# Performance work log

Measured on AMD Instinct MI355X. Metric: run time of the kernel, lower is better.

Reference implementation:

```python
import jax, jax.numpy as jnp
import numpy as np

ELEMENTS = (1, 6, 7, 8)
SIGMA = 3.0
NTRANSFORMS = 2


def fwht(x):
    """Fast Walsh-Hadamard transform over the last axis (unnormalized, d power of 2)."""
    d = x.shape[-1]
    lead = x.shape[:-1]
    x = x.reshape((-1, d))
    h = 1
    while h < d:
        x = x.reshape((-1, d // (2 * h), 2, h))
        a, b = x[..., 0, :], x[..., 1, :]
        x = jnp.stack((a + b, a - b), axis=-2).reshape((-1, d))
        h *= 2
    return x.reshape(lead + (d,))


def sorf(sub, D):
    """SORF: repeated (normalized Hadamard) @ (diag(D_t) x). sub [..., p], D [T, s, p] -> [..., s, p]."""
    d = sub.shape[-1]
    hnorm = 1.0 / jnp.sqrt(jnp.asarray(d, sub.dtype))
    x = sub[..., None, :]  # broadcast over nstacks
    for t in range(D.shape[0]):
        x = fwht(D[t] * x) * hnorm
    return x


def setup_inputs() -> dict:
    key = jax.random.key(0)
    k1, k2, k3, k4, k5, k6 = jax.random.split(key, 6)
    nmols, natoms, rep_dim = 256, 32, 256
    n_elem, npcas, nstacks = 4, 128, 32
    nfeat = npcas * nstacks
    rep = jax.random.normal(k1, (nmols, natoms, rep_dim), dtype=jnp.float32)
    # charges: 0 = padding atom (matches no element), else one of ELEMENTS
    idx = jax.random.randint(k2, (nmols, natoms), 0, 5)
    Z = jnp.asarray([0, 1, 6, 7, 8], dtype=jnp.int32)[idx]
    reductors = 0.05 * jax.random.normal(k3, (n_elem, rep_dim, npcas), dtype=jnp.float32)
    # Rademacher +-1 diagonals, as in get_SORF_diagonals
    Dmat = jnp.where(jax.random.uniform(k4, (n_elem, NTRANSFORMS, nstacks, npcas)) >= 0.5, 1.0, -1.0).astype(jnp.float32)
    bias = 2.0 * jnp.pi * jax.random.uniform(k5, (n_elem, nfeat), dtype=jnp.float32)
    alpha = jax.random.normal(k6, (nfeat,), dtype=jnp.float32)
    return {"rep": rep, "Z": Z, "reductors": reductors, "Dmat": Dmat, "bias": bias, "alpha": alpha}


def reference(rep, Z, reductors, Dmat, bias, alpha):
    nmols = rep.shape[0]
    npcas = Dmat.shape[-1]
    nfeat = Dmat.shape[2] * npcas  # nstacks * npcas
    coeff_norm = jnp.sqrt(jnp.asarray(npcas, rep.dtype)) / SIGMA
    feat_norm = jnp.sqrt(jnp.asarray(2.0 / nfeat, rep.dtype))
    Ztest = jnp.zeros((nmols, nfeat), dtype=rep.dtype)
    for ei, e in enumerate(ELEMENTS):
        mask = (Z == e).astype(rep.dtype)                       # [m, a]
        sub = jnp.einsum('mar,rp->map', rep, reductors[ei])     # project_representation
        coeffs = coeff_norm * sorf(sub, Dmat[ei])               # [m, a, s, p]
        feats = feat_norm * jnp.cos(coeffs.reshape(nmols, -1, nfeat) + bias[ei])
        Ztest = Ztest + jnp.einsum('ma,maf->mf', mask, feats)   # masked scatter-add per molecule
    return Ztest @ alpha  # total_energies [m]
```

## Files before the change

kernel.cpp:

```cpp
#include <hip/hip_runtime.h>

#define NMOLS   256
#define NATOMS  32
#define REPD    256
#define NPCAS   128
#define NSTACKS 32
#define NFEAT   4096
#define NELEM   4

#define LIST_OFF 0
#define META_OFF 32768
#define SUB_OFF  40960

#define SCALE_C 0.029462782549439476f
#define FEATN_C 0.022097086912079608f

__device__ __forceinline__ int elem_of(int z) {
  return (z == 1) ? 0 : (z == 6) ? 1 : (z == 7) ? 2 : (z == 8) ? 3 : -1;
}

__global__ __launch_bounds__(256) void k0_bucket(const int* __restrict__ Z,
                                                 int* __restrict__ list,
                                                 int* __restrict__ meta,
                                                 float* __restrict__ out) {
  __shared__ int4 cntS[256];
  const int t = threadIdx.x;
  out[t] = 0.0f;
  int c0 = 0, c1 = 0, c2 = 0, c3 = 0;
  #pragma unroll
  for (int k = 0; k < 32; ++k) {
    const int z = Z[k * 256 + t];
    c0 += (z == 1); c1 += (z == 6); c2 += (z == 7); c3 += (z == 8);
  }
  int4 v = make_int4(c0, c1, c2, c3);
  cntS[t] = v;
  __syncthreads();
  for (int step = 1; step < 256; step <<= 1) {
    int4 add = make_int4(0, 0, 0, 0);
    if (t >= step) add = cntS[t - step];
    __syncthreads();
    v.x += add.x; v.y += add.y; v.z += add.z; v.w += add.w;
    cntS[t] = v;
    __syncthreads();
  }
  const int4 tot = cntS[255];
  int o0 = v.x - c0;
  int o1 = tot.x + v.y - c1;
  int o2 = tot.x + tot.y + v.z - c2;
  int o3 = tot.x + tot.y + tot.z + v.w - c3;
  #pragma unroll
  for (int k = 0; k < 32; ++k) {
    const int a = k * 256 + t;
    const int z = Z[a];
    if      (z == 1) list[o0++] = a;
    else if (z == 6) list[o1++] = a;
    else if (z == 7) list[o2++] = a;
    else if (z == 8) list[o3++] = a;
  }
  if (t == 0) {
    meta[0] = tot.x; meta[1] = tot.y; meta[2] = tot.z; meta[3] = tot.w;
    meta[4] = 0;
    meta[5] = tot.x;
    meta[6] = tot.x + tot.y;
    meta[7] = tot.x + tot.y + tot.z;
    meta[8] = tot.x + tot.y + tot.z + tot.w;
  }
}

__global__ __launch_bounds__(256) void k1_matvec(const float* __restrict__ rep,
                                                 const float* __restrict__ reductors,
                                                 const int* __restrict__ list,
                                                 const int* __restrict__ meta,
                                                 float* __restrict__ sub) {
  const int e = blockIdx.y;
  const int cnt = meta[e];
  const int off = meta[4 + e];
  const int start = blockIdx.x * 64;
  if (start >= cnt) return;
  const int n = min(64, cnt - start);
  const int t = threadIdx.x;

  __shared__ int aidS[64];
  __shared__ float repS[64][128];

  if (t < 64) aidS[t] = list[off + start + (t < n ? t : 0)];

  const int pq = t & 31, jq = t >> 5;
  const int p0 = pq * 4, j0 = jq * 8;
  const float* red_e = reductors + e * (REPD * NPCAS);

  float acc[8][4];
  #pragma unroll
  for (int j = 0; j < 8; ++j)
    #pragma unroll
    for (int q = 0; q < 4; ++q) acc[j][q] = 0.0f;

  for (int kh = 0; kh < 2; ++kh) {
    __syncthreads();
    #pragma unroll
    for (int it = 0; it < 8; ++it) {
      const int idx = it * 256 + t;
      const int row = idx >> 5;
      const int q   = idx & 31;
      *(float4*)&repS[row][q * 4] =
          *(const float4*)(rep + (size_t)aidS[row] * 256 + kh * 128 + q * 4);
    }
    __syncthreads();

    const float* redk = red_e + (kh * 128) * 128 + p0;
    for (int r0 = 0; r0 < 128; r0 += 4) {
      const float4 rv0 = *(const float4*)(redk + (r0 + 0) * 128);
      const float4 rv1 = *(const float4*)(redk + (r0 + 1) * 128);
      const float4 rv2 = *(const float4*)(redk + (r0 + 2) * 128);
      const float4 rv3 = *(const float4*)(redk + (r0 + 3) * 128);
      float4 rp[8];
      #pragma unroll
      for (int j = 0; j < 8; ++j)
        rp[j] = *(const float4*)&repS[j0 + j][r0];
      #pragma unroll
      for (int j = 0; j < 8; ++j) {
        acc[j][0] = fmaf(rp[j].w, rv3.x, fmaf(rp[j].z, rv2.x, fmaf(rp[j].y, rv1.x, fmaf(rp[j].x, rv0.x, acc[j][0]))));
        acc[j][1] = fmaf(rp[j].w, rv3.y, fmaf(rp[j].z, rv2.y, fmaf(rp[j].y, rv1.y, fmaf(rp[j].x, rv0.y, acc[j][1]))));
        acc[j][2] = fmaf(rp[j].w, rv3.z, fmaf(rp[j].z, rv2.z, fmaf(rp[j].y, rv1.z, fmaf(rp[j].x, rv0.z, acc[j][2]))));
        acc[j][3] = fmaf(rp[j].w, rv3.w, fmaf(rp[j].z, rv2.w, fmaf(rp[j].y, rv1.w, fmaf(rp[j].x, rv0.w, acc[j][3]))));
      }
    }
  }

  #pragma unroll
  for (int j = 0; j < 8; ++j) {
    const int a = j0 + j;
    if (a < n) {
      float4 v = make_float4(acc[j][0], acc[j][1], acc[j][2], acc[j][3]);
      *(float4*)(sub + (size_t)(off + start + a) * 128 + p0) = v;
    }
  }
}

template <int CTRL>
__device__ __forceinline__ float dppx(float x) {
  return __int_as_float(__builtin_amdgcn_update_dpp(0, __float_as_int(x), CTRL, 0xF, 0xF, true));
}
template <int OFF>
__device__ __forceinline__ float swzx(float x) {
  return __int_as_float(__builtin_amdgcn_ds_swizzle(__float_as_int(x), OFF));
}

#define BFLY_DPP(x, CTRL, sg) { float t_ = dppx<CTRL>(x); (x) = fmaf((x), (sg), t_); }
#define BFLY_SWZ(x, OFF, sg)  { float t_ = swzx<OFF>(x);  (x) = fmaf((x), (sg), t_); }

#define SWAP16(a, b) asm("v_permlane16_swap_b32 %0, %1" : "+v"(a), "+v"(b));
#define SWAP32(a, b) asm("v_permlane32_swap_b32 %0, %1" : "+v"(a), "+v"(b));
#define XST16(lo, hi) { SWAP16(lo, hi) float s_ = (lo) + (hi), d_ = (lo) - (hi); SWAP16(s_, d_) (lo) = s_; (hi) = d_; }
#define XST32(lo, hi) { SWAP32(lo, hi) float s_ = (lo) + (hi), d_ = (lo) - (hi); SWAP32(s_, d_) (lo) = s_; (hi) = d_; }

#define FW128(lo, hi) { \
  { float a_ = (lo) + (hi), b_ = (lo) - (hi); (lo) = a_; (hi) = b_; } \
  BFLY_DPP(lo, 0xB1, sg1)    BFLY_DPP(hi, 0xB1, sg1) \
  BFLY_DPP(lo, 0x4E, sg2)    BFLY_DPP(hi, 0x4E, sg2) \
  BFLY_SWZ(lo, 0x101F, sg4)  BFLY_SWZ(hi, 0x101F, sg4) \
  BFLY_DPP(lo, 0x128, sg8)   BFLY_DPP(hi, 0x128, sg8) \
  XST16(lo, hi) \
  XST32(lo, hi) }

__global__ __launch_bounds__(256) void k2_features(const float* __restrict__ sub,
                                                   const int* __restrict__ list,
                                                   const int* __restrict__ meta,
                                                   const int* __restrict__ Z,
                                                   const float* __restrict__ Dmat,
                                                   const float* __restrict__ bias,
                                                   const float* __restrict__ alpha,
                                                   float* __restrict__ out) {
  const int total = meta[8];
  const int w = threadIdx.x >> 6, lane = threadIdx.x & 63;
  const int pos0 = blockIdx.x * 16 + w * 4;
  if (pos0 >= total) return;
  const bool has1 = (pos0 + 1) < total;
  const bool has2 = (pos0 + 2) < total;
  const bool has3 = (pos0 + 3) < total;

  const float sg1 = (lane & 1) ? -1.0f : 1.0f;
  const float sg2 = (lane & 2) ? -1.0f : 1.0f;
  const float sg4 = (lane & 4) ? -1.0f : 1.0f;
  const float sg8 = (lane & 8) ? -1.0f : 1.0f;

  const int aid0 = list[pos0];
  const int e0 = elem_of(Z[aid0]);
  const float slo0 = sub[(size_t)pos0 * 128 + lane];
  const float shi0 = sub[(size_t)pos0 * 128 + 64 + lane];

  int aid1 = aid0, e1 = 0; float slo1 = 0.0f, shi1 = 0.0f;
  if (has1) {
    aid1 = list[pos0 + 1]; e1 = elem_of(Z[aid1]);
    slo1 = sub[(size_t)(pos0 + 1) * 128 + lane];
    shi1 = sub[(size_t)(pos0 + 1) * 128 + 64 + lane];
  }
  int aid2 = aid0, e2 = 0; float slo2 = 0.0f, shi2 = 0.0f;
  if (has2) {
    aid2 = list[pos0 + 2]; e2 = elem_of(Z[aid2]);
    slo2 = sub[(size_t)(pos0 + 2) * 128 + lane];
    shi2 = sub[(size_t)(pos0 + 2) * 128 + 64 + lane];
  }
  int aid3 = aid0, e3 = 0; float slo3 = 0.0f, shi3 = 0.0f;
  if (has3) {
    aid3 = list[pos0 + 3]; e3 = elem_of(Z[aid3]);
    slo3 = sub[(size_t)(pos0 + 3) * 128 + lane];
    shi3 = sub[(size_t)(pos0 + 3) * 128 + 64 + lane];
  }

  const float* De0 = Dmat + e0 * (2 * NSTACKS * NPCAS);
  const float* De1 = Dmat + e1 * (2 * NSTACKS * NPCAS);
  const float* De2 = Dmat + e2 * (2 * NSTACKS * NPCAS);
  const float* De3 = Dmat + e3 * (2 * NSTACKS * NPCAS);
  const float* be0 = bias + e0 * NFEAT;
  const float* be1 = bias + e1 * NFEAT;
  const float* be2 = bias + e2 * NFEAT;
  const float* be3 = bias + e3 * NFEAT;

  float acc0 = 0.0f, acc1 = 0.0f, acc2 = 0.0f, acc3 = 0.0f;

  for (int s = 0; s < NSTACKS; ++s) {
    const int s0 = s * 128, s1 = (NSTACKS + s) * 128;
    const float alo = alpha[s0 + lane], ahi = alpha[s0 + 64 + lane];

    float lo0 = slo0 * De0[s0 + lane], hi0 = shi0 * De0[s0 + 64 + lane];
    float lo1 = slo1 * De1[s0 + lane], hi1 = shi1 * De1[s0 + 64 + lane];
    float lo2 = slo2 * De2[s0 + lane], hi2 = shi2 * De2[s0 + 64 + lane];
    float lo3 = slo3 * De3[s0 + lane], hi3 = shi3 * De3[s0 + 64 + lane];

    FW128(lo0, hi0) FW128(lo1, hi1) FW128(lo2, hi2) FW128(lo3, hi3)

    lo0 *= De0[s1 + lane]; hi0 *= De0[s1 + 64 + lane];
    lo1 *= De1[s1 + lane]; hi1 *= De1[s1 + 64 + lane];
    lo2 *= De2[s1 + lane]; hi2 *= De2[s1 + 64 + lane];
    lo3 *= De3[s1 + lane]; hi3 *= De3[s1 + 64 + lane];

    FW128(lo0, hi0) FW128(lo1, hi1) FW128(lo2, hi2) FW128(lo3, hi3)

    acc0 = fmaf(__cosf(fmaf(lo0, SCALE_C, be0[s0 + lane])),      alo, acc0);
    acc0 = fmaf(__cosf(fmaf(hi0, SCALE_C, be0[s0 + 64 + lane])), ahi, acc0);
    acc1 = fmaf(__cosf(fmaf(lo1, SCALE_C, be1[s0 + lane])),      alo, acc1);
    acc1 = fmaf(__cosf(fmaf(hi1, SCALE_C, be1[s0 + 64 + lane])), ahi, acc1);
    acc2 = fmaf(__cosf(fmaf(lo2, SCALE_C, be2[s0 + lane])),      alo, acc2);
    acc2 = fmaf(__cosf(fmaf(hi2, SCALE_C, be2[s0 + 64 + lane])), ahi, acc2);
    acc3 = fmaf(__cosf(fmaf(lo3, SCALE_C, be3[s0 + lane])),      alo, acc3);
    acc3 = fmaf(__cosf(fmaf(hi3, SCALE_C, be3[s0 + 64 + lane])), ahi, acc3);
  }

  #pragma unroll
  for (int o = 32; o > 0; o >>= 1) {
    acc0 += __shfl_xor(acc0, o, 64);
    acc1 += __shfl_xor(acc1, o, 64);
    acc2 += __shfl_xor(acc2, o, 64);
    acc3 += __shfl_xor(acc3, o, 64);
  }
  if (lane == 0)         atomicAdd(out + (aid0 >> 5), acc0 * FEATN_C);
  if (lane == 1 && has1) atomicAdd(out + (aid1 >> 5), acc1 * FEATN_C);
  if (lane == 2 && has2) atomicAdd(out + (aid2 >> 5), acc2 * FEATN_C);
  if (lane == 3 && has3) atomicAdd(out + (aid3 >> 5), acc3 * FEATN_C);
}

extern "C" void kernel_launch(void* const* d_in, const int* in_sizes, int n_in,
                              void* d_out, int out_size, void* d_ws, size_t ws_size,
                              hipStream_t stream) {
  const float* rep       = (const float*)d_in[0];
  const int*   Z         = (const int*)  d_in[1];
  const float* reductors = (const float*)d_in[2];
  const float* Dmat      = (const float*)d_in[3];
  const float* bias      = (const float*)d_in[4];
  const float* alpha     = (const float*)d_in[5];
  float* out = (float*)d_out;

  char* wsb = (char*)d_ws;
  int*   list = (int*)(wsb + LIST_OFF);
  int*   meta = (int*)(wsb + META_OFF);
  float* sub  = (float*)(wsb + SUB_OFF);

  k0_bucket<<<1, 256, 0, stream>>>(Z, list, meta, out);
  dim3 g1(32, 4);
  k1_matvec<<<g1, 256, 0, stream>>>(rep, reductors, list, meta, sub);
  k2_features<<<512, 256, 0, stream>>>(sub, list, meta, Z, Dmat, bias, alpha, out);
}
```

Measured before the change: 83.13 us.

## Shrink matvec and feature blocks to spread work across more CUs

The projection kernel now handles 8 atoms per block with one accumulator row per thread instead of 64 atoms with 8x4 register tiles, and launches 1024x4 blocks. The feature kernel drops to one 64-thread wavefront per block with 2048 blocks. The aim is to fill more compute units and cut per-block latency for a small problem, at the cost of reading the reductor matrix many more times and launching more tiny blocks.

```diff
diff --git a/kernel.cpp b/kernel.cpp
--- a/kernel.cpp
+++ b/kernel.cpp
@@ -75,65 +75,47 @@
   const int e = blockIdx.y;
   const int cnt = meta[e];
   const int off = meta[4 + e];
-  const int start = blockIdx.x * 64;
+  const int start = blockIdx.x * 8;
   if (start >= cnt) return;
-  const int n = min(64, cnt - start);
+  const int n = min(8, cnt - start);
   const int t = threadIdx.x;
 
-  __shared__ int aidS[64];
-  __shared__ float repS[64][128];
-
-  if (t < 64) aidS[t] = list[off + start + (t < n ? t : 0)];
+  __shared__ int aidS[8];
+  __shared__ float repS[8][256];
+
+  if (t < 8) aidS[t] = list[off + start + (t < n ? t : 0)];
+  __syncthreads();
+
+  #pragma unroll
+  for (int it = 0; it < 2; ++it) {
+    const int idx = it * 256 + t;
+    const int row = idx >> 6;
+    const int q   = idx & 63;
+    *(float4*)&repS[row][q * 4] = *(const float4*)(rep + (size_t)aidS[row] * 256 + q * 4);
+  }
+  __syncthreads();
 
   const int pq = t & 31, jq = t >> 5;
-  const int p0 = pq * 4, j0 = jq * 8;
-  const float* red_e = reductors + e * (REPD * NPCAS);
-
-  float acc[8][4];
-  #pragma unroll
-  for (int j = 0; j < 8; ++j)
-    #pragma unroll
-    for (int q = 0; q < 4; ++q) acc[j][q] = 0.0f;
-
-  for (int kh = 0; kh < 2; ++kh) {
-    __syncthreads();
-    #pragma unroll
-    for (int it = 0; it < 8; ++it) {
-      const int idx = it * 256 + t;
-      const int row = idx >> 5;
-      const int q   = idx & 31;
-      *(float4*)&repS[row][q * 4] =
-          *(const float4*)(rep + (size_t)aidS[row] * 256 + kh * 128 + q * 4);
-    }
-    __syncthreads();
-
-    const float* redk = red_e + (kh * 128) * 128 + p0;
-    for (int r0 = 0; r0 < 128; r0 += 4) {
-      const float4 rv0 = *(const float4*)(redk + (r0 + 0) * 128);
-      const float4 rv1 = *(const float4*)(redk + (r0 + 1) * 128);
-      const float4 rv2 = *(const float4*)(redk + (r0 + 2) * 128);
-      const float4 rv3 = *(const float4*)(redk + (r0 + 3) * 128);
-      float4 rp[8];
-      #pragma unroll
-      for (int j = 0; j < 8; ++j)
-        rp[j] = *(const float4*)&repS[j0 + j][r0];
-      #pragma unroll
-      for (int j = 0; j < 8; ++j) {
-        acc[j][0] = fmaf(rp[j].w, rv3.x, fmaf(rp[j].z, rv2.x, fmaf(rp[j].y, rv1.x, fmaf(rp[j].x, rv0.x, acc[j][0]))));
-        acc[j][1] = fmaf(rp[j].w, rv3.y, fmaf(rp[j].z, rv2.y, fmaf(rp[j].y, rv1.y, fmaf(rp[j].x, rv0.y, acc[j][1]))));
-        acc[j][2] = fmaf(rp[j].w, rv3.z, fmaf(rp[j].z, rv2.z, fmaf(rp[j].y, rv1.z, fmaf(rp[j].x, rv0.z, acc[j][2]))));
-        acc[j][3] = fmaf(rp[j].w, rv3.w, fmaf(rp[j].z, rv2.w, fmaf(rp[j].y, rv1.w, fmaf(rp[j].x, rv0.w, acc[j][3]))));
-      }
-    }
-  }
-
-  #pragma unroll
-  for (int j = 0; j < 8; ++j) {
-    const int a = j0 + j;
-    if (a < n) {
-      float4 v = make_float4(acc[j][0], acc[j][1], acc[j][2], acc[j][3]);
-      *(float4*)(sub + (size_t)(off + start + a) * 128 + p0) = v;
-    }
+  const int p0 = pq * 4;
+  const float* red_e = reductors + e * (REPD * NPCAS) + p0;
+
+  float a0 = 0.0f, a1 = 0.0f, a2 = 0.0f, a3 = 0.0f;
+
+  for (int r0 = 0; r0 < 256; r0 += 4) {
+    const float4 rv0 = *(const float4*)(red_e + (r0 + 0) * 128);
+    const float4 rv1 = *(const float4*)(red_e + (r0 + 1) * 128);
+    const float4 rv2 = *(const float4*)(red_e + (r0 + 2) * 128);
+    const float4 rv3 = *(const float4*)(red_e + (r0 + 3) * 128);
+    const float4 q4  = *(const float4*)&repS[jq][r0];
+    a0 = fmaf(q4.w, rv3.x, fmaf(q4.z, rv2.x, fmaf(q4.y, rv1.x, fmaf(q4.x, rv0.x, a0))));
+    a1 = fmaf(q4.w, rv3.y, fmaf(q4.z, rv2.y, fmaf(q4.y, rv1.y, fmaf(q4.x, rv0.y, a1))));
+    a2 = fmaf(q4.w, rv3.z, fmaf(q4.z, rv2.z, fmaf(q4.y, rv1.z, fmaf(q4.x, rv0.z, a2))));
+    a3 = fmaf(q4.w, rv3.w, fmaf(q4.z, rv2.w, fmaf(q4.y, rv1.w, fmaf(q4.x, rv0.w, a3))));
+  }
+
+  if (jq < n) {
+    float4 v = make_float4(a0, a1, a2, a3);
+    *(float4*)(sub + (size_t)(off + start + jq) * 128 + p0) = v;
   }
 }
 
@@ -163,17 +145,17 @@
   XST16(lo, hi) \
   XST32(lo, hi) }
 
-__global__ __launch_bounds__(256) void k2_features(const float* __restrict__ sub,
-                                                   const int* __restrict__ list,
-                                                   const int* __restrict__ meta,
-                                                   const int* __restrict__ Z,
-                                                   const float* __restrict__ Dmat,
-                                                   const float* __restrict__ bias,
-                                                   const float* __restrict__ alpha,
-                                                   float* __restrict__ out) {
+__global__ __launch_bounds__(64) void k2_features(const float* __restrict__ sub,
+                                                  const int* __restrict__ list,
+                                                  const int* __restrict__ meta,
+                                                  const int* __restrict__ Z,
+                                                  const float* __restrict__ Dmat,
+                                                  const float* __restrict__ bias,
+                                                  const float* __restrict__ alpha,
+                                                  float* __restrict__ out) {
   const int total = meta[8];
-  const int w = threadIdx.x >> 6, lane = threadIdx.x & 63;
-  const int pos0 = blockIdx.x * 16 + w * 4;
+  const int lane = threadIdx.x & 63;
+  const int pos0 = blockIdx.x * 4;
   if (pos0 >= total) return;
   const bool has1 = (pos0 + 1) < total;
   const bool has2 = (pos0 + 2) < total;
@@ -277,7 +259,7 @@
   float* sub  = (float*)(wsb + SUB_OFF);
 
   k0_bucket<<<1, 256, 0, stream>>>(Z, list, meta, out);
-  dim3 g1(32, 4);
+  dim3 g1(1024, 4);
   k1_matvec<<<g1, 256, 0, stream>>>(rep, reductors, list, meta, sub);
-  k2_features<<<512, 256, 0, stream>>>(sub, list, meta, Z, Dmat, bias, alpha, out);
-}
+  k2_features<<<2048, 64, 0, stream>>>(sub, list, meta, Z, Dmat, bias, alpha, out);
+}
```

After: 104.1 us. 1.25x slower.
